# Kernel optimization log

Hardware: AMD Instinct MI355X
Metric: run time of the kernel (lower is better)

Reference implementation:

```python
import jax, jax.numpy as jnp
import numpy as np

N_NODES = 50000
N_EDGES = 800000
IN_DIM = 16
HID = 16
EDGE_DIM = 8
GRAPH_DIM = 8
OUT_DIM = 1
N_LAYERS = 3


def setup_inputs() -> dict:
    key = jax.random.key(0)
    ks = jax.random.split(key, 12)
    x = jax.random.normal(ks[0], (N_NODES, IN_DIM), dtype=jnp.float32)
    edge_index = jax.random.randint(ks[1], (2, N_EDGES), 0, N_NODES, dtype=jnp.int32)
    edge_attr = jax.random.normal(ks[2], (N_EDGES, EDGE_DIM), dtype=jnp.float32)
    graph_features = jax.random.normal(ks[3], (GRAPH_DIM, N_NODES), dtype=jnp.float32)
    # stacked per-layer params (all layers have in=hidden=16)
    nnW = jax.random.normal(ks[4], (N_LAYERS, EDGE_DIM, IN_DIM * HID), dtype=jnp.float32) * 0.1
    nnb = jax.random.normal(ks[5], (N_LAYERS, IN_DIM * HID), dtype=jnp.float32) * 0.1
    rootW = jax.random.normal(ks[6], (N_LAYERS, IN_DIM, HID), dtype=jnp.float32) * 0.1
    bias = jax.random.normal(ks[7], (N_LAYERS, HID), dtype=jnp.float32) * 0.1
    head_W = jax.random.normal(ks[8], (HID + GRAPH_DIM, OUT_DIM), dtype=jnp.float32) * 0.1
    head_b = jax.random.normal(ks[9], (OUT_DIM,), dtype=jnp.float32) * 0.1
    return {"x": x, "edge_index": edge_index, "edge_attr": edge_attr,
            "graph_features": graph_features, "nnW": nnW, "nnb": nnb,
            "rootW": rootW, "bias": bias, "head_W": head_W, "head_b": head_b}


def _nnconv(x, src, dst, edge_attr, nnW, nnb, rootW, bias):
    # edge MLP -> per-edge weight matrix [E, in, out]
    theta = (edge_attr @ nnW + nnb).reshape(-1, x.shape[1], rootW.shape[1])
    # per-edge matmul with gathered source features, scatter-add to targets
    msg = jnp.einsum('ei,eio->eo', x[src], theta)  # [E, out]
    agg = jax.ops.segment_sum(msg, dst, num_segments=N_NODES)
    return agg + x @ rootW + bias


def reference(x, edge_index, edge_attr, graph_features, nnW, nnb, rootW, bias, head_W, head_b):
    src, dst = edge_index[0], edge_index[1]
    for i in range(N_LAYERS):
        x = _nnconv(x, src, dst, edge_attr, nnW[i], nnb[i], rootW[i], bias[i])
        x = jax.nn.relu(x)
        # dropout p=0.0 / eval mode -> identity
    h = jnp.concatenate([x, graph_features.T], axis=1)  # [N, hid+graph_dim]
    return h @ head_W + head_b
```

## Files before the change

### kernel.cpp

```cpp
#include <hip/hip_runtime.h>
#include <hip/hip_fp16.h>

#define N_NODES 50000
#define N_EDGES 800000
#define IN_DIM 16
#define HID 16
#define EDGE_DIM 8
#define GRAPH_DIM 8
#define N_LAYERS 3
#define HIST_BLOCKS ((N_EDGES + 255) / 256)
#define PREP_BLOCKS ((N_NODES * HID + 255) / 256)
#define SCAN_BS 256
#define SCAN_NB ((N_NODES + SCAN_BS - 1) / SCAN_BS)

typedef unsigned uint4v __attribute__((ext_vector_type(4)));

struct Rec { unsigned e0, e1, e2, e3; int src; int pad; };

__device__ __forceinline__ unsigned pack_h2(float lo, float hi) {
    __half2 h = __floats2half2_rn(lo, hi);
    return *reinterpret_cast<unsigned*>(&h);
}
__device__ __forceinline__ float2 unpack_h2(unsigned u) {
    __half2 h = *reinterpret_cast<__half2*>(&u);
    return __half22float2(h);
}

__device__ __forceinline__ void prep_one(int t, const float* __restrict__ x_in,
                                         const float* __restrict__ nnW,
                                         const float* __restrict__ nnb,
                                         const float* __restrict__ rootW,
                                         const float* __restrict__ bias,
                                         unsigned* __restrict__ zw_h,
                                         float* __restrict__ rb, int apply_relu) {
    int n = t >> 4;
    int o = t & 15;

    float xv[IN_DIM];
    const float* xr = x_in + n * IN_DIM;
#pragma unroll
    for (int i = 0; i < IN_DIM; ++i) {
        float v = xr[i];
        xv[i] = apply_relu ? fmaxf(v, 0.0f) : v;
    }

    float zk[EDGE_DIM];
#pragma unroll
    for (int k = 0; k < EDGE_DIM; ++k) zk[k] = 0.0f;
    float wv = 0.0f;
    float rv = bias[o];

#pragma unroll
    for (int i = 0; i < IN_DIM; ++i) {
        float xi = xv[i];
#pragma unroll
        for (int k = 0; k < EDGE_DIM; ++k) {
            zk[k] = fmaf(xi, nnW[k * 256 + i * 16 + o], zk[k]);
        }
        wv = fmaf(xi, nnb[i * 16 + o], wv);
        rv = fmaf(xi, rootW[i * 16 + o], rv);
    }

    unsigned* zn = zw_h + (size_t)n * 80;
#pragma unroll
    for (int kp = 0; kp < 4; ++kp) zn[kp * 16 + o] = pack_h2(zk[2 * kp], zk[2 * kp + 1]);
    zn[64 + o] = pack_h2(wv, 0.0f);
    rb[n * 16 + o] = rv;
}

__global__ __launch_bounds__(256)
void hist_prep0_kernel(const int* __restrict__ ei, int* __restrict__ deg,
                       const float* __restrict__ x, const float* __restrict__ nnW,
                       const float* __restrict__ nnb, const float* __restrict__ rootW,
                       const float* __restrict__ bias,
                       unsigned* __restrict__ zw_h, float* __restrict__ rb) {
    if (blockIdx.x < HIST_BLOCKS) {
        int e = blockIdx.x * 256 + threadIdx.x;
        if (e < N_EDGES) atomicAdd(&deg[ei[N_EDGES + e]], 1);
    } else {
        int t = (blockIdx.x - HIST_BLOCKS) * 256 + threadIdx.x;
        if (t < N_NODES * HID)
            prep_one(t, x, nnW, nnb, rootW, bias, zw_h, rb, 0);
    }
}

__global__ __launch_bounds__(SCAN_BS)
void scan1_kernel(const int* __restrict__ deg, int* __restrict__ offs,
                  int* __restrict__ bsum) {
    __shared__ int s[SCAN_BS];
    int tid = threadIdx.x;
    int i = blockIdx.x * SCAN_BS + tid;
    int v = (i < N_NODES) ? deg[i] : 0;
    s[tid] = v;
    __syncthreads();
    for (int off = 1; off < SCAN_BS; off <<= 1) {
        int t = (tid >= off) ? s[tid - off] : 0;
        __syncthreads();
        s[tid] += t;
        __syncthreads();
    }
    if (i < N_NODES) offs[i] = s[tid] - v;
    if (tid == SCAN_BS - 1) bsum[blockIdx.x] = s[tid];
}

__global__ __launch_bounds__(SCAN_BS)
void scan23_kernel(int* __restrict__ offs, const int* __restrict__ bsum,
                   int* __restrict__ deg) {
    __shared__ int s[SCAN_BS];
    int tid = threadIdx.x;
    s[tid] = (tid < (int)blockIdx.x) ? bsum[tid] : 0;
    __syncthreads();
    for (int off = SCAN_BS / 2; off > 0; off >>= 1) {
        if (tid < off) s[tid] += s[tid + off];
        __syncthreads();
    }
    int base = s[0];
    int i = blockIdx.x * SCAN_BS + tid;
    if (i < N_NODES) {
        int o = offs[i] + base;
        offs[i] = o;
        deg[i] = o;
    }
    if (i == 0) offs[N_NODES] = N_EDGES;
}

__global__ __launch_bounds__(256)
void fill_kernel(const int* __restrict__ ei, const float* __restrict__ ea,
                 int* __restrict__ cur, Rec* __restrict__ csr) {
    int e = blockIdx.x * blockDim.x + threadIdx.x;
    if (e >= N_EDGES) return;
    int src = ei[e];
    int dst = ei[N_EDGES + e];
    const float4* eap = (const float4*)(ea + (size_t)e * EDGE_DIM);
    float4 e0 = eap[0];
    float4 e1 = eap[1];
    Rec r;
    r.e0 = pack_h2(e0.x, e0.y);
    r.e1 = pack_h2(e0.z, e0.w);
    r.e2 = pack_h2(e1.x, e1.y);
    r.e3 = pack_h2(e1.z, e1.w);
    r.src = src;
    r.pad = 0;
    int j = atomicAdd(&cur[dst], 1);
    csr[j] = r;
}

__global__ __launch_bounds__(256)
void prep_kernel(const float* __restrict__ x_in, const float* __restrict__ nnW,
                 const float* __restrict__ nnb, const float* __restrict__ rootW,
                 const float* __restrict__ bias,
                 unsigned* __restrict__ zw_h, float* __restrict__ rb) {
    int t = blockIdx.x * blockDim.x + threadIdx.x;
    if (t < N_NODES * HID)
        prep_one(t, x_in, nnW, nnb, rootW, bias, zw_h, rb, 1);
}

__device__ __forceinline__ void edge_accum(const unsigned* __restrict__ zp,
                                           uint4v rec, int o, float& acc) {
    unsigned q0 = zp[o];
    unsigned q1 = zp[16 + o];
    unsigned q2 = zp[32 + o];
    unsigned q3 = zp[48 + o];
    unsigned q4 = zp[64 + o];
    float2 e01 = unpack_h2(rec.x);
    float2 e23 = unpack_h2(rec.y);
    float2 e45 = unpack_h2(rec.z);
    float2 e67 = unpack_h2(rec.w);
    float2 z01 = unpack_h2(q0);
    float2 z23 = unpack_h2(q1);
    float2 z45 = unpack_h2(q2);
    float2 z67 = unpack_h2(q3);
    float2 w_  = unpack_h2(q4);
    acc += w_.x;
    acc = fmaf(e01.x, z01.x, acc);
    acc = fmaf(e01.y, z01.y, acc);
    acc = fmaf(e23.x, z23.x, acc);
    acc = fmaf(e23.y, z23.y, acc);
    acc = fmaf(e45.x, z45.x, acc);
    acc = fmaf(e45.y, z45.y, acc);
    acc = fmaf(e67.x, z67.x, acc);
    acc = fmaf(e67.y, z67.y, acc);
}

template <bool DO_HEAD>
__global__ __launch_bounds__(256)
void agg_kernel(const int* __restrict__ offs,
                const Rec* __restrict__ csr,
                const unsigned* __restrict__ zw_h,
                float* __restrict__ buf,
                const float* __restrict__ gf,
                const float* __restrict__ hW,
                const float* __restrict__ hb,
                float* __restrict__ out) {
    int tid = threadIdx.x;
    int o = tid & 15;
    int n = blockIdx.x * 16 + (tid >> 4);
    if (n >= N_NODES) return;

    float acc0 = buf[n * HID + o];
    float acc1 = 0.0f;
    int jb = offs[n], je = offs[n + 1];
    int j = jb;
    for (; j + 1 < je; j += 2) {
        Rec r0 = csr[j];
        Rec r1 = csr[j + 1];
        uint4v a0 = {r0.e0, r0.e1, r0.e2, r0.e3};
        uint4v a1 = {r1.e0, r1.e1, r1.e2, r1.e3};
        edge_accum(zw_h + (size_t)r0.src * 80, a0, o, acc0);
        edge_accum(zw_h + (size_t)r1.src * 80, a1, o, acc1);
    }
    if (j < je) {
        Rec r0 = csr[j];
        uint4v a0 = {r0.e0, r0.e1, r0.e2, r0.e3};
        edge_accum(zw_h + (size_t)r0.src * 80, a0, o, acc0);
    }
    float acc = acc0 + acc1;

    if (!DO_HEAD) {
        buf[n * HID + o] = acc;
    } else {
        float h = fmaxf(acc, 0.0f) * hW[o];
        if (o < GRAPH_DIM) h = fmaf(gf[o * N_NODES + n], hW[HID + o], h);
#pragma unroll
        for (int off = 8; off > 0; off >>= 1) h += __shfl_xor(h, off, 16);
        if (o == 0) out[n] = h + hb[0];
    }
}

extern "C" void kernel_launch(void* const* d_in, const int* in_sizes, int n_in,
                              void* d_out, int out_size, void* d_ws, size_t ws_size,
                              hipStream_t stream) {
    const float* x     = (const float*)d_in[0];
    const int*   ei    = (const int*)d_in[1];
    const float* ea    = (const float*)d_in[2];
    const float* gf    = (const float*)d_in[3];
    const float* nnW   = (const float*)d_in[4];
    const float* nnb   = (const float*)d_in[5];
    const float* rootW = (const float*)d_in[6];
    const float* bias  = (const float*)d_in[7];
    const float* hW    = (const float*)d_in[8];
    const float* hb    = (const float*)d_in[9];
    float* out = (float*)d_out;

    unsigned* zw_h = (unsigned*)d_ws;
    Rec* csr   = (Rec*)(zw_h + (size_t)N_NODES * 80);
    float* bufA = (float*)((char*)csr + (size_t)N_EDGES * sizeof(Rec));
    float* bufB = bufA + (size_t)N_NODES * HID;
    int* deg    = (int*)(bufB + (size_t)N_NODES * HID);
    int* offs   = deg + N_NODES;
    int* bsum   = offs + N_NODES + 8;

    dim3 blk(256);
    dim3 grid_e(HIST_BLOCKS);
    dim3 grid_hp(HIST_BLOCKS + PREP_BLOCKS);
    dim3 grid_no(PREP_BLOCKS);
    dim3 grid_a((N_NODES + 15) / 16);

    hipMemsetAsync(deg, 0, N_NODES * sizeof(int), stream);
    hist_prep0_kernel<<<grid_hp, blk, 0, stream>>>(ei, deg, x, nnW, nnb, rootW, bias,
                                                   zw_h, bufA);
    scan1_kernel<<<SCAN_NB, SCAN_BS, 0, stream>>>(deg, offs, bsum);
    scan23_kernel<<<SCAN_NB, SCAN_BS, 0, stream>>>(offs, bsum, deg);
    fill_kernel<<<grid_e, blk, 0, stream>>>(ei, ea, deg, csr);

    agg_kernel<false><<<grid_a, blk, 0, stream>>>(offs, csr, zw_h, bufA,
                                                  nullptr, nullptr, nullptr, nullptr);
    prep_kernel<<<grid_no, blk, 0, stream>>>(bufA, nnW + 2048, nnb + 256,
                                             rootW + 256, bias + 16, zw_h, bufB);
    agg_kernel<false><<<grid_a, blk, 0, stream>>>(offs, csr, zw_h, bufB,
                                                  nullptr, nullptr, nullptr, nullptr);
    prep_kernel<<<grid_no, blk, 0, stream>>>(bufB, nnW + 4096, nnb + 512,
                                             rootW + 512, bias + 32, zw_h, bufA);
    agg_kernel<true><<<grid_a, blk, 0, stream>>>(offs, csr, zw_h, bufA,
                                                 gf, hW, hb, out);
}
```

Measured before the change: 370.2 us.

## Fuse next-layer prep into aggregation kernel with double-buffered node tables

The aggregation kernel can now compute the next layer's per-node projections (z, w, root+bias) directly from its aggregated result. It gathers the 16 hidden values via wave shuffles, applies ReLU, and writes to a second zw buffer, which removes the separate prep kernels and the round trip of the hidden state through global memory. Double-buffering zw avoids read/write races between layers but needs more workspace, and the old path is kept as a fallback when the workspace is too small. The fused kernel also does more work per thread, which may lower occupancy for the gather-heavy aggregation.

```diff
diff --git a/kernel.cpp b/kernel.cpp
--- a/kernel.cpp
+++ b/kernel.cpp
@@ -7,7 +7,6 @@
 #define HID 16
 #define EDGE_DIM 8
 #define GRAPH_DIM 8
-#define N_LAYERS 3
 #define HIST_BLOCKS ((N_EDGES + 255) / 256)
 #define PREP_BLOCKS ((N_NODES * HID + 255) / 256)
 #define SCAN_BS 256
@@ -24,6 +23,35 @@
 __device__ __forceinline__ float2 unpack_h2(unsigned u) {
     __half2 h = *reinterpret_cast<__half2*>(&u);
     return __half22float2(h);
+}
+
+__device__ __forceinline__ void prep_core(const float* __restrict__ xv, int n, int o,
+                                          const float* __restrict__ nnW,
+                                          const float* __restrict__ nnb,
+                                          const float* __restrict__ rootW,
+                                          const float* __restrict__ bias,
+                                          unsigned* __restrict__ zw_h,
+                                          float* __restrict__ rb) {
+    float zk[EDGE_DIM];
+#pragma unroll
+    for (int k = 0; k < EDGE_DIM; ++k) zk[k] = 0.0f;
+    float wv = 0.0f;
+    float rv = bias[o];
+#pragma unroll
+    for (int i = 0; i < IN_DIM; ++i) {
+        float xi = xv[i];
+#pragma unroll
+        for (int k = 0; k < EDGE_DIM; ++k) {
+            zk[k] = fmaf(xi, nnW[k * 256 + i * 16 + o], zk[k]);
+        }
+        wv = fmaf(xi, nnb[i * 16 + o], wv);
+        rv = fmaf(xi, rootW[i * 16 + o], rv);
+    }
+    unsigned* zn = zw_h + (size_t)n * 80;
+#pragma unroll
+    for (int kp = 0; kp < 4; ++kp) zn[kp * 16 + o] = pack_h2(zk[2 * kp], zk[2 * kp + 1]);
+    zn[64 + o] = pack_h2(wv, 0.0f);
+    rb[n * 16 + o] = rv;
 }
 
 __device__ __forceinline__ void prep_one(int t, const float* __restrict__ x_in,
@@ -35,7 +63,6 @@
                                          float* __restrict__ rb, int apply_relu) {
     int n = t >> 4;
     int o = t & 15;
-
     float xv[IN_DIM];
     const float* xr = x_in + n * IN_DIM;
 #pragma unroll
@@ -43,29 +70,7 @@
         float v = xr[i];
         xv[i] = apply_relu ? fmaxf(v, 0.0f) : v;
     }
-
-    float zk[EDGE_DIM];
-#pragma unroll
-    for (int k = 0; k < EDGE_DIM; ++k) zk[k] = 0.0f;
-    float wv = 0.0f;
-    float rv = bias[o];
-
-#pragma unroll
-    for (int i = 0; i < IN_DIM; ++i) {
-        float xi = xv[i];
-#pragma unroll
-        for (int k = 0; k < EDGE_DIM; ++k) {
-            zk[k] = fmaf(xi, nnW[k * 256 + i * 16 + o], zk[k]);
-        }
-        wv = fmaf(xi, nnb[i * 16 + o], wv);
-        rv = fmaf(xi, rootW[i * 16 + o], rv);
-    }
-
-    unsigned* zn = zw_h + (size_t)n * 80;
-#pragma unroll
-    for (int kp = 0; kp < 4; ++kp) zn[kp * 16 + o] = pack_h2(zk[2 * kp], zk[2 * kp + 1]);
-    zn[64 + o] = pack_h2(wv, 0.0f);
-    rb[n * 16 + o] = rv;
+    prep_core(xv, n, o, nnW, nnb, rootW, bias, zw_h, rb);
 }
 
 __global__ __launch_bounds__(256)
@@ -182,12 +187,18 @@
     acc = fmaf(e67.y, z67.y, acc);
 }
 
-template <bool DO_HEAD>
+template <int MODE>
 __global__ __launch_bounds__(256)
 void agg_kernel(const int* __restrict__ offs,
                 const Rec* __restrict__ csr,
                 const unsigned* __restrict__ zw_h,
                 float* __restrict__ buf,
+                unsigned* __restrict__ zw_next,
+                float* __restrict__ rb_next,
+                const float* __restrict__ nnW,
+                const float* __restrict__ nnb,
+                const float* __restrict__ rootW,
+                const float* __restrict__ bias,
                 const float* __restrict__ gf,
                 const float* __restrict__ hW,
                 const float* __restrict__ hb,
@@ -216,8 +227,17 @@
     }
     float acc = acc0 + acc1;
 
-    if (!DO_HEAD) {
+    if (MODE == 0) {
         buf[n * HID + o] = acc;
+    } else if (MODE == 1) {
+        int lane_base = (tid & 63) & ~15;
+        float xv[IN_DIM];
+#pragma unroll
+        for (int i = 0; i < IN_DIM; ++i) {
+            float v = __shfl(acc, lane_base + i, 64);
+            xv[i] = fmaxf(v, 0.0f);
+        }
+        prep_core(xv, n, o, nnW, nnb, rootW, bias, zw_next, rb_next);
     } else {
         float h = fmaxf(acc, 0.0f) * hW[o];
         if (o < GRAPH_DIM) h = fmaf(gf[o * N_NODES + n], hW[HID + o], h);
@@ -242,35 +262,75 @@
     const float* hb    = (const float*)d_in[9];
     float* out = (float*)d_out;
 
-    unsigned* zw_h = (unsigned*)d_ws;
-    Rec* csr   = (Rec*)(zw_h + (size_t)N_NODES * 80);
-    float* bufA = (float*)((char*)csr + (size_t)N_EDGES * sizeof(Rec));
-    float* bufB = bufA + (size_t)N_NODES * HID;
-    int* deg    = (int*)(bufB + (size_t)N_NODES * HID);
-    int* offs   = deg + N_NODES;
-    int* bsum   = offs + N_NODES + 8;
-
     dim3 blk(256);
     dim3 grid_e(HIST_BLOCKS);
     dim3 grid_hp(HIST_BLOCKS + PREP_BLOCKS);
     dim3 grid_no(PREP_BLOCKS);
     dim3 grid_a((N_NODES + 15) / 16);
 
-    hipMemsetAsync(deg, 0, N_NODES * sizeof(int), stream);
-    hist_prep0_kernel<<<grid_hp, blk, 0, stream>>>(ei, deg, x, nnW, nnb, rootW, bias,
-                                                   zw_h, bufA);
-    scan1_kernel<<<SCAN_NB, SCAN_BS, 0, stream>>>(deg, offs, bsum);
-    scan23_kernel<<<SCAN_NB, SCAN_BS, 0, stream>>>(offs, bsum, deg);
-    fill_kernel<<<grid_e, blk, 0, stream>>>(ei, ea, deg, csr);
-
-    agg_kernel<false><<<grid_a, blk, 0, stream>>>(offs, csr, zw_h, bufA,
+    const size_t need_fused = (size_t)N_NODES * 80 * 4 * 2
+                            + (size_t)N_EDGES * sizeof(Rec)
+                            + (size_t)N_NODES * HID * 4 * 2
+                            + (size_t)(N_NODES * 2 + 64) * 4;
+
+    if (ws_size >= need_fused) {
+        unsigned* zw0 = (unsigned*)d_ws;
+        unsigned* zw1 = zw0 + (size_t)N_NODES * 80;
+        Rec* csr   = (Rec*)(zw1 + (size_t)N_NODES * 80);
+        float* bufA = (float*)((char*)csr + (size_t)N_EDGES * sizeof(Rec));
+        float* bufB = bufA + (size_t)N_NODES * HID;
+        int* deg    = (int*)(bufB + (size_t)N_NODES * HID);
+        int* offs   = deg + N_NODES;
+        int* bsum   = offs + N_NODES + 8;
+
+        hipMemsetAsync(deg, 0, N_NODES * sizeof(int), stream);
+        hist_prep0_kernel<<<grid_hp, blk, 0, stream>>>(ei, deg, x, nnW, nnb, rootW,
+                                                       bias, zw0, bufA);
+        scan1_kernel<<<SCAN_NB, SCAN_BS, 0, stream>>>(deg, offs, bsum);
+        scan23_kernel<<<SCAN_NB, SCAN_BS, 0, stream>>>(offs, bsum, deg);
+        fill_kernel<<<grid_e, blk, 0, stream>>>(ei, ea, deg, csr);
+
+        agg_kernel<1><<<grid_a, blk, 0, stream>>>(offs, csr, zw0, bufA, zw1, bufB,
+                                                  nnW + 2048, nnb + 256, rootW + 256,
+                                                  bias + 16,
                                                   nullptr, nullptr, nullptr, nullptr);
-    prep_kernel<<<grid_no, blk, 0, stream>>>(bufA, nnW + 2048, nnb + 256,
-                                             rootW + 256, bias + 16, zw_h, bufB);
-    agg_kernel<false><<<grid_a, blk, 0, stream>>>(offs, csr, zw_h, bufB,
+        agg_kernel<1><<<grid_a, blk, 0, stream>>>(offs, csr, zw1, bufB, zw0, bufA,
+                                                  nnW + 4096, nnb + 512, rootW + 512,
+                                                  bias + 32,
                                                   nullptr, nullptr, nullptr, nullptr);
-    prep_kernel<<<grid_no, blk, 0, stream>>>(bufB, nnW + 4096, nnb + 512,
-                                             rootW + 512, bias + 32, zw_h, bufA);
-    agg_kernel<true><<<grid_a, blk, 0, stream>>>(offs, csr, zw_h, bufA,
-                                                 gf, hW, hb, out);
-}
+        agg_kernel<2><<<grid_a, blk, 0, stream>>>(offs, csr, zw0, bufA,
+                                                  nullptr, nullptr, nullptr, nullptr,
+                                                  nullptr, nullptr, gf, hW, hb, out);
+    } else {
+        unsigned* zw0 = (unsigned*)d_ws;
+        Rec* csr   = (Rec*)(zw0 + (size_t)N_NODES * 80);
+        float* bufA = (float*)((char*)csr + (size_t)N_EDGES * sizeof(Rec));
+        float* bufB = bufA + (size_t)N_NODES * HID;
+        int* deg    = (int*)(bufB + (size_t)N_NODES * HID);
+        int* offs   = deg + N_NODES;
+        int* bsum   = offs + N_NODES + 8;
+
+        hipMemsetAsync(deg, 0, N_NODES * sizeof(int), stream);
+        hist_prep0_kernel<<<grid_hp, blk, 0, stream>>>(ei, deg, x, nnW, nnb, rootW,
+                                                       bias, zw0, bufA);
+        scan1_kernel<<<SCAN_NB, SCAN_BS, 0, stream>>>(deg, offs, bsum);
+        scan23_kernel<<<SCAN_NB, SCAN_BS, 0, stream>>>(offs, bsum, deg);
+        fill_kernel<<<grid_e, blk, 0, stream>>>(ei, ea, deg, csr);
+
+        agg_kernel<0><<<grid_a, blk, 0, stream>>>(offs, csr, zw0, bufA,
+                                                  nullptr, nullptr, nullptr, nullptr,
+                                                  nullptr, nullptr,
+                                                  nullptr, nullptr, nullptr, nullptr);
+        prep_kernel<<<grid_no, blk, 0, stream>>>(bufA, nnW + 2048, nnb + 256,
+                                                 rootW + 256, bias + 16, zw0, bufB);
+        agg_kernel<0><<<grid_a, blk, 0, stream>>>(offs, csr, zw0, bufB,
+                                                  nullptr, nullptr, nullptr, nullptr,
+                                                  nullptr, nullptr,
+                                                  nullptr, nullptr, nullptr, nullptr);
+        prep_kernel<<<grid_no, blk, 0, stream>>>(bufB, nnW + 4096, nnb + 512,
+                                                 rootW + 512, bias + 32, zw0, bufA);
+        agg_kernel<2><<<grid_a, blk, 0, stream>>>(offs, csr, zw0, bufA,
+                                                  nullptr, nullptr, nullptr, nullptr,
+                                                  nullptr, nullptr, gf, hW, hb, out);
+    }
+}
```

New measurement: 348.3 us. -5.9%, faster.
